# Kernel tuning notes

Hardware: AMD Instinct MI355X
Metric: run time of the kernel (lower is better)

## Reference

```python
import jax, jax.numpy as jnp
import numpy as np

B, N, U = 16, 1024, 64  # batch, nodes, num_units
ALPHA = 0.2  # LeakyReLU negative slope
NEG = -9e15


def setup_inputs() -> dict:
    key = jax.random.key(0)
    ks = jax.random.split(key, 7)
    X = jax.random.normal(ks[0], (B, N, U), dtype=jnp.float32)
    state = jax.random.normal(ks[1], (B, N, U), dtype=jnp.float32)
    # random sparse adjacency (avg degree ~32) with self-loops
    adj = (jax.random.uniform(ks[2], (N, N)) < 32.0 / N).astype(jnp.float32)
    adj = jnp.maximum(adj, jnp.eye(N, dtype=jnp.float32))
    def xavier(k, shape):
        fan_in, fan_out = shape
        s = 1.414 * np.sqrt(6.0 / (fan_in + fan_out))
        return jax.random.uniform(k, shape, jnp.float32, -s, s)
    W1 = xavier(ks[3], (2 * U, 2 * U))   # gat_1: in 2U -> out 2U
    a1 = xavier(ks[4], (4 * U, 1))       # attention vector, 2*out
    W2 = xavier(ks[5], (2 * U, U))       # gat_2: in 2U -> out U
    a2 = xavier(ks[6], (2 * U, 1))
    return {"X": X, "state": state, "adj": adj, "W1": W1, "a1": a1, "W2": W2, "a2": a2}


def _gat_layer(x, adj, W, a):
    # x: [b,n,f_in], W: [f_in,F], a: [2F,1]
    h = jnp.einsum('bnf,fo->bno', x, W)              # [b,n,F]
    F_out = W.shape[1]
    s_src = h @ a[:F_out, 0]                         # [b,n] contribution of node i
    s_dst = h @ a[F_out:, 0]                         # [b,n] contribution of node j
    e = jax.nn.leaky_relu(s_src[:, :, None] + s_dst[:, None, :], ALPHA)  # [b,n,n]
    e = jnp.where(adj[None, :, :] > 0, e, NEG)
    att = jax.nn.softmax(e, axis=2)                  # masked softmax over neighbors j
    return jnp.einsum('bij,bjf->bif', att, h)        # [b,n,F]


def reference(X, state, adj, W1, a1, W2, a2):
    X1 = jnp.concatenate([X, state], axis=2)         # [b,n,2U]
    gv = jax.nn.sigmoid(_gat_layer(X1, adj, W1, a1)) # [b,n,2U]
    r, z = jnp.split(gv, 2, axis=2)                  # each [b,n,U]
    X2 = jnp.concatenate([X, r * state], axis=2)
    h_t1 = jnp.tanh(_gat_layer(X2, adj, W2, a2))     # [b,n,U]
    new_h = z * state + (1.0 - z) * h_t1
    return new_h
```

## Files before the change

### kernel.cpp

```cpp
#include <hip/hip_runtime.h>

#define BB 16
#define NN 1024
#define UU 64
#define LALPHA 0.2f
#define MAXD 192

__global__ void build_csr(const float* __restrict__ adj, int* __restrict__ deg,
                          int* __restrict__ cols) {
    __shared__ int cnt;
    int i = blockIdx.x;
    if (threadIdx.x == 0) cnt = 0;
    __syncthreads();
    for (int j = threadIdx.x; j < NN; j += blockDim.x) {
        if (adj[(size_t)i * NN + j] > 0.0f) {
            int p = atomicAdd(&cnt, 1);
            if (p < MAXD) cols[(size_t)i * MAXD + p] = j;
        }
    }
    __syncthreads();
    if (threadIdx.x == 0) deg[i] = cnt < MAXD ? cnt : MAXD;
}

template <int FOUT, int RPG, int GROUPS>
__global__ void gemm_concat(const float* __restrict__ A0, const float* __restrict__ A1,
                            const float* __restrict__ W, float* __restrict__ out) {
    const int TR = RPG * GROUPS;
    __shared__ float xs[TR][129];
    int t = threadIdx.x;
    int f = t % FOUT;
    int rg = t / FOUT;
    int base = blockIdx.x * TR;
    for (int idx = t; idx < TR * 128; idx += FOUT * GROUPS) {
        int r = idx >> 7, c = idx & 127;
        xs[r][c] = (c < 64) ? A0[(size_t)(base + r) * 64 + c]
                            : A1[(size_t)(base + r) * 64 + (c - 64)];
    }
    __syncthreads();
    float acc[RPG];
#pragma unroll
    for (int rr = 0; rr < RPG; rr++) acc[rr] = 0.f;
    for (int k = 0; k < 128; k++) {
        float w = W[(size_t)k * FOUT + f];
#pragma unroll
        for (int rr = 0; rr < RPG; rr++) acc[rr] += xs[rg * RPG + rr][k] * w;
    }
#pragma unroll
    for (int rr = 0; rr < RPG; rr++)
        out[(size_t)(base + rg * RPG + rr) * FOUT + f] = acc[rr];
}

template <int F>
__global__ void score_kernel(const float* __restrict__ h, const float* __restrict__ a,
                             float* __restrict__ s_src, float* __restrict__ s_dst) {
    int m = blockIdx.x, lane = threadIdx.x;
    float ps = 0.f, pd = 0.f;
    for (int f = lane; f < F; f += 64) {
        float hv = h[(size_t)m * F + f];
        ps += hv * a[f];
        pd += hv * a[F + f];
    }
#pragma unroll
    for (int o = 32; o >= 1; o >>= 1) {
        ps += __shfl_xor(ps, o);
        pd += __shfl_xor(pd, o);
    }
    if (lane == 0) {
        s_src[m] = ps;
        s_dst[m] = pd;
    }
}

__global__ void attn1_kernel(const int* __restrict__ deg, const int* __restrict__ cols,
                             const float* __restrict__ h1, const float* __restrict__ s_src,
                             const float* __restrict__ s_dst, const float* __restrict__ state,
                             float* __restrict__ rstate, float* __restrict__ zbuf) {
    int bi = blockIdx.x;
    int i = bi & (NN - 1);
    int b = bi >> 10;
    int lane = threadIdx.x;
    int d = deg[i];
    const int* cl = cols + (size_t)i * MAXD;
    float ssrc = s_src[bi];
    __shared__ float w[MAXD];
    float mx = -1e30f;
    for (int j = lane; j < d; j += 64) {
        float e = ssrc + s_dst[b * NN + cl[j]];
        e = e > 0.f ? e : LALPHA * e;
        w[j] = e;
        mx = fmaxf(mx, e);
    }
#pragma unroll
    for (int o = 32; o >= 1; o >>= 1) mx = fmaxf(mx, __shfl_xor(mx, o));
    float sum = 0.f;
    for (int j = lane; j < d; j += 64) {
        float e = __expf(w[j] - mx);
        w[j] = e;
        sum += e;
    }
#pragma unroll
    for (int o = 32; o >= 1; o >>= 1) sum += __shfl_xor(sum, o);
    float inv = 1.f / sum;
    float acc0 = 0.f, acc1 = 0.f;
    for (int j = 0; j < d; j++) {
        float wj = w[j];
        const float* hr = h1 + (size_t)(b * NN + cl[j]) * 128;
        acc0 += wj * hr[lane];
        acc1 += wj * hr[lane + 64];
    }
    float rg = 1.f / (1.f + __expf(-acc0 * inv));
    float zg = 1.f / (1.f + __expf(-acc1 * inv));
    float st = state[(size_t)bi * 64 + lane];
    rstate[(size_t)bi * 64 + lane] = rg * st;
    zbuf[(size_t)bi * 64 + lane] = zg;
}

__global__ void attn2_kernel(const int* __restrict__ deg, const int* __restrict__ cols,
                             const float* __restrict__ h2, const float* __restrict__ s_src,
                             const float* __restrict__ s_dst, const float* __restrict__ state,
                             const float* __restrict__ zbuf, float* __restrict__ out) {
    int bi = blockIdx.x;
    int i = bi & (NN - 1);
    int b = bi >> 10;
    int lane = threadIdx.x;
    int d = deg[i];
    const int* cl = cols + (size_t)i * MAXD;
    float ssrc = s_src[bi];
    __shared__ float w[MAXD];
    float mx = -1e30f;
    for (int j = lane; j < d; j += 64) {
        float e = ssrc + s_dst[b * NN + cl[j]];
        e = e > 0.f ? e : LALPHA * e;
        w[j] = e;
        mx = fmaxf(mx, e);
    }
#pragma unroll
    for (int o = 32; o >= 1; o >>= 1) mx = fmaxf(mx, __shfl_xor(mx, o));
    float sum = 0.f;
    for (int j = lane; j < d; j += 64) {
        float e = __expf(w[j] - mx);
        w[j] = e;
        sum += e;
    }
#pragma unroll
    for (int o = 32; o >= 1; o >>= 1) sum += __shfl_xor(sum, o);
    float inv = 1.f / sum;
    float acc = 0.f;
    for (int j = 0; j < d; j++) {
        acc += w[j] * h2[(size_t)(b * NN + cl[j]) * 64 + lane];
    }
    float ht = tanhf(acc * inv);
    float z = zbuf[(size_t)bi * 64 + lane];
    float st = state[(size_t)bi * 64 + lane];
    out[(size_t)bi * 64 + lane] = z * st + (1.f - z) * ht;
}

extern "C" void kernel_launch(void* const* d_in, const int* in_sizes, int n_in,
                              void* d_out, int out_size, void* d_ws, size_t ws_size,
                              hipStream_t stream) {
    const float* X     = (const float*)d_in[0];
    const float* state = (const float*)d_in[1];
    const float* adj   = (const float*)d_in[2];
    const float* W1    = (const float*)d_in[3];
    const float* a1    = (const float*)d_in[4];
    const float* W2    = (const float*)d_in[5];
    const float* a2    = (const float*)d_in[6];
    float* out = (float*)d_out;

    char* ws = (char*)d_ws;
    size_t off = 0;
    auto alloc = [&](size_t bytes) -> void* {
        void* p = ws + off;
        off = (off + bytes + 255) & ~(size_t)255;
        return p;
    };
    int*   deg    = (int*)alloc(NN * sizeof(int));
    int*   cols   = (int*)alloc((size_t)NN * MAXD * sizeof(int));
    float* h1     = (float*)alloc((size_t)BB * NN * 128 * sizeof(float));
    float* ssrc1  = (float*)alloc((size_t)BB * NN * sizeof(float));
    float* sdst1  = (float*)alloc((size_t)BB * NN * sizeof(float));
    float* rstate = (float*)alloc((size_t)BB * NN * 64 * sizeof(float));
    float* zbuf   = (float*)alloc((size_t)BB * NN * 64 * sizeof(float));
    float* h2     = (float*)alloc((size_t)BB * NN * 64 * sizeof(float));
    float* ssrc2  = (float*)alloc((size_t)BB * NN * sizeof(float));
    float* sdst2  = (float*)alloc((size_t)BB * NN * sizeof(float));

    const int M = BB * NN;

    build_csr<<<NN, 256, 0, stream>>>(adj, deg, cols);
    gemm_concat<128, 8, 2><<<M / 16, 256, 0, stream>>>(X, state, W1, h1);
    score_kernel<128><<<M, 64, 0, stream>>>(h1, a1, ssrc1, sdst1);
    attn1_kernel<<<M, 64, 0, stream>>>(deg, cols, h1, ssrc1, sdst1, state, rstate, zbuf);
    gemm_concat<64, 4, 4><<<M / 16, 256, 0, stream>>>(X, rstate, W2, h2);
    score_kernel<64><<<M, 64, 0, stream>>>(h2, a2, ssrc2, sdst2);
    attn2_kernel<<<M, 64, 0, stream>>>(deg, cols, h2, ssrc2, sdst2, state, zbuf, out);
}
```

Baseline: 148.5 us.

## Fuse attention scores into register-tiled GEMM and stage neighbor lists in LDS

Replaces the per-row GEMM and the separate score kernels with one register-tiled 4x4 GEMM that uses float4 loads and computes s_src/s_dst in its epilogue through shuffle reductions. This drops two kernel launches and a re-read of h. The attention kernels now copy the neighbor column list into shared memory and unroll the weighted gather by two to keep more loads in flight. The cost is more registers in the GEMM and extra barriers in the attention kernels.

```diff
diff --git a/kernel.cpp b/kernel.cpp
--- a/kernel.cpp
+++ b/kernel.cpp
@@ -2,7 +2,6 @@
 
 #define BB 16
 #define NN 1024
-#define UU 64
 #define LALPHA 0.2f
 #define MAXD 192
 
@@ -22,52 +21,69 @@
     if (threadIdx.x == 0) deg[i] = cnt < MAXD ? cnt : MAXD;
 }
 
-template <int FOUT, int RPG, int GROUPS>
-__global__ void gemm_concat(const float* __restrict__ A0, const float* __restrict__ A1,
-                            const float* __restrict__ W, float* __restrict__ out) {
-    const int TR = RPG * GROUPS;
-    __shared__ float xs[TR][129];
+template <int FOUT, int RB>
+__global__ void gemm_score(const float* __restrict__ A0, const float* __restrict__ A1,
+                           const float* __restrict__ W, const float* __restrict__ avec,
+                           float* __restrict__ h, float* __restrict__ s_src,
+                           float* __restrict__ s_dst) {
+    constexpr int TFN = FOUT / 4;
+    constexpr int NT = (RB / 4) * TFN;
+    __shared__ float xs[RB][132];
     int t = threadIdx.x;
-    int f = t % FOUT;
-    int rg = t / FOUT;
-    int base = blockIdx.x * TR;
-    for (int idx = t; idx < TR * 128; idx += FOUT * GROUPS) {
-        int r = idx >> 7, c = idx & 127;
-        xs[r][c] = (c < 64) ? A0[(size_t)(base + r) * 64 + c]
-                            : A1[(size_t)(base + r) * 64 + (c - 64)];
-    }
-    __syncthreads();
-    float acc[RPG];
-#pragma unroll
-    for (int rr = 0; rr < RPG; rr++) acc[rr] = 0.f;
-    for (int k = 0; k < 128; k++) {
-        float w = W[(size_t)k * FOUT + f];
-#pragma unroll
-        for (int rr = 0; rr < RPG; rr++) acc[rr] += xs[rg * RPG + rr][k] * w;
-    }
-#pragma unroll
-    for (int rr = 0; rr < RPG; rr++)
-        out[(size_t)(base + rg * RPG + rr) * FOUT + f] = acc[rr];
-}
-
-template <int F>
-__global__ void score_kernel(const float* __restrict__ h, const float* __restrict__ a,
-                             float* __restrict__ s_src, float* __restrict__ s_dst) {
-    int m = blockIdx.x, lane = threadIdx.x;
-    float ps = 0.f, pd = 0.f;
-    for (int f = lane; f < F; f += 64) {
-        float hv = h[(size_t)m * F + f];
-        ps += hv * a[f];
-        pd += hv * a[F + f];
-    }
-#pragma unroll
-    for (int o = 32; o >= 1; o >>= 1) {
-        ps += __shfl_xor(ps, o);
-        pd += __shfl_xor(pd, o);
-    }
-    if (lane == 0) {
-        s_src[m] = ps;
-        s_dst[m] = pd;
+    int tf = t % TFN, tr = t / TFN;
+    int f0 = tf * 4, r0 = tr * 4;
+    int base = blockIdx.x * RB;
+
+    for (int idx = t; idx < RB * 32; idx += NT) {
+        int r = idx >> 5, c = (idx & 31) * 4;
+        float4 v = (c < 64) ? *(const float4*)(A0 + (size_t)(base + r) * 64 + c)
+                            : *(const float4*)(A1 + (size_t)(base + r) * 64 + (c - 64));
+        xs[r][c] = v.x; xs[r][c + 1] = v.y; xs[r][c + 2] = v.z; xs[r][c + 3] = v.w;
+    }
+    __syncthreads();
+
+    float acc[4][4] = {};
+    for (int k = 0; k < 128; k += 4) {
+        float4 xv[4], wv[4];
+#pragma unroll
+        for (int i = 0; i < 4; i++) xv[i] = *(const float4*)&xs[r0 + i][k];
+#pragma unroll
+        for (int i = 0; i < 4; i++) wv[i] = *(const float4*)(W + (size_t)(k + i) * FOUT + f0);
+#pragma unroll
+        for (int i = 0; i < 4; i++) {
+            float xr[4] = {xv[i].x, xv[i].y, xv[i].z, xv[i].w};
+#pragma unroll
+            for (int kk = 0; kk < 4; kk++) {
+                acc[i][0] += xr[kk] * wv[kk].x;
+                acc[i][1] += xr[kk] * wv[kk].y;
+                acc[i][2] += xr[kk] * wv[kk].z;
+                acc[i][3] += xr[kk] * wv[kk].w;
+            }
+        }
+    }
+
+    float a_s[4], a_d[4];
+#pragma unroll
+    for (int i = 0; i < 4; i++) {
+        a_s[i] = avec[f0 + i];
+        a_d[i] = avec[FOUT + f0 + i];
+    }
+#pragma unroll
+    for (int i = 0; i < 4; i++) {
+        int m = base + r0 + i;
+        *(float4*)(h + (size_t)m * FOUT + f0) =
+            make_float4(acc[i][0], acc[i][1], acc[i][2], acc[i][3]);
+        float ps = acc[i][0] * a_s[0] + acc[i][1] * a_s[1] + acc[i][2] * a_s[2] + acc[i][3] * a_s[3];
+        float pd = acc[i][0] * a_d[0] + acc[i][1] * a_d[1] + acc[i][2] * a_d[2] + acc[i][3] * a_d[3];
+#pragma unroll
+        for (int o = TFN / 2; o >= 1; o >>= 1) {
+            ps += __shfl_xor(ps, o);
+            pd += __shfl_xor(pd, o);
+        }
+        if (tf == 0) {
+            s_src[m] = ps;
+            s_dst[m] = pd;
+        }
     }
 }
 
@@ -80,9 +96,11 @@
     int b = bi >> 10;
     int lane = threadIdx.x;
     int d = deg[i];
-    const int* cl = cols + (size_t)i * MAXD;
     float ssrc = s_src[bi];
     __shared__ float w[MAXD];
+    __shared__ int cl[MAXD];
+    for (int j = lane; j < d; j += 64) cl[j] = cols[(size_t)i * MAXD + j];
+    __syncthreads();
     float mx = -1e30f;
     for (int j = lane; j < d; j += 64) {
         float e = ssrc + s_dst[b * NN + cl[j]];
@@ -100,13 +118,24 @@
     }
 #pragma unroll
     for (int o = 32; o >= 1; o >>= 1) sum += __shfl_xor(sum, o);
+    __syncthreads();
     float inv = 1.f / sum;
     float acc0 = 0.f, acc1 = 0.f;
-    for (int j = 0; j < d; j++) {
-        float wj = w[j];
-        const float* hr = h1 + (size_t)(b * NN + cl[j]) * 128;
-        acc0 += wj * hr[lane];
-        acc1 += wj * hr[lane + 64];
+    int j = 0;
+    for (; j + 1 < d; j += 2) {
+        float w0 = w[j], w1 = w[j + 1];
+        const float* p0 = h1 + (size_t)(b * NN + cl[j]) * 128;
+        const float* p1 = h1 + (size_t)(b * NN + cl[j + 1]) * 128;
+        float x0 = p0[lane], y0 = p0[lane + 64];
+        float x1 = p1[lane], y1 = p1[lane + 64];
+        acc0 += w0 * x0 + w1 * x1;
+        acc1 += w0 * y0 + w1 * y1;
+    }
+    if (j < d) {
+        float w0 = w[j];
+        const float* p0 = h1 + (size_t)(b * NN + cl[j]) * 128;
+        acc0 += w0 * p0[lane];
+        acc1 += w0 * p0[lane + 64];
     }
     float rg = 1.f / (1.f + __expf(-acc0 * inv));
     float zg = 1.f / (1.f + __expf(-acc1 * inv));
@@ -124,9 +153,11 @@
     int b = bi >> 10;
     int lane = threadIdx.x;
     int d = deg[i];
-    const int* cl = cols + (size_t)i * MAXD;
     float ssrc = s_src[bi];
     __shared__ float w[MAXD];
+    __shared__ int cl[MAXD];
+    for (int j = lane; j < d; j += 64) cl[j] = cols[(size_t)i * MAXD + j];
+    __syncthreads();
     float mx = -1e30f;
     for (int j = lane; j < d; j += 64) {
         float e = ssrc + s_dst[b * NN + cl[j]];
@@ -144,11 +175,17 @@
     }
 #pragma unroll
     for (int o = 32; o >= 1; o >>= 1) sum += __shfl_xor(sum, o);
+    __syncthreads();
     float inv = 1.f / sum;
     float acc = 0.f;
-    for (int j = 0; j < d; j++) {
-        acc += w[j] * h2[(size_t)(b * NN + cl[j]) * 64 + lane];
-    }
+    int j = 0;
+    for (; j + 1 < d; j += 2) {
+        float w0 = w[j], w1 = w[j + 1];
+        const float* p0 = h2 + (size_t)(b * NN + cl[j]) * 64;
+        const float* p1 = h2 + (size_t)(b * NN + cl[j + 1]) * 64;
+        acc += w0 * p0[lane] + w1 * p1[lane];
+    }
+    if (j < d) acc += w[j] * h2[(size_t)(b * NN + cl[j]) * 64 + lane];
     float ht = tanhf(acc * inv);
     float z = zbuf[(size_t)bi * 64 + lane];
     float st = state[(size_t)bi * 64 + lane];
@@ -188,10 +225,8 @@
     const int M = BB * NN;
 
     build_csr<<<NN, 256, 0, stream>>>(adj, deg, cols);
-    gemm_concat<128, 8, 2><<<M / 16, 256, 0, stream>>>(X, state, W1, h1);
-    score_kernel<128><<<M, 64, 0, stream>>>(h1, a1, ssrc1, sdst1);
+    gemm_score<128, 32><<<M / 32, 256, 0, stream>>>(X, state, W1, a1, h1, ssrc1, sdst1);
     attn1_kernel<<<M, 64, 0, stream>>>(deg, cols, h1, ssrc1, sdst1, state, rstate, zbuf);
-    gemm_concat<64, 4, 4><<<M / 16, 256, 0, stream>>>(X, rstate, W2, h2);
-    score_kernel<64><<<M, 64, 0, stream>>>(h2, a2, ssrc2, sdst2);
+    gemm_score<64, 64><<<M / 64, 256, 0, stream>>>(X, rstate, W2, a2, h2, ssrc2, sdst2);
     attn2_kernel<<<M, 64, 0, stream>>>(deg, cols, h2, ssrc2, sdst2, state, zbuf, out);
 }
```

Result: faster. 141.9 us (-4.5%).
